# Kernel optimization log

Measured on AMD Instinct MI355X. Metric: run time of the kernel, lower is better.

## Reference

```python
import jax, jax.numpy as jnp
import numpy as np

B, T, D, V, L = 32, 1000, 768, 31, 200  # batch, frames, feat dim, vocab (blank=0), max target len
NEG = -1e30  # log-domain 'zero'


def setup_inputs() -> dict:
    key = jax.random.key(0)
    ks = jax.random.split(key, 5)
    pred = jax.random.normal(ks[0], (B, T, D), jnp.float32)
    targets = jax.random.randint(ks[1], (B * L,), 1, V)            # flat labels, blank(0) excluded
    input_lengths = jax.random.randint(ks[2], (B,), 800, T + 1)
    target_lengths = jax.random.randint(ks[3], (B,), 150, L + 1)
    W = jax.random.normal(ks[4], (V, D), jnp.float32) * 0.02       # ctc_head weight
    b = jnp.zeros((V,), jnp.float32)                               # ctc_head bias
    return dict(pred=pred, targets=targets, input_lengths=input_lengths,
                target_lengths=target_lengths, W=W, b=b)


def _ctc_loss(log_probs, tgt2d, in_len, tgt_len):
    """log_probs: (B,T,V); tgt2d: (B,L) padded labels; mean CTC loss (torch semantics,
    blank=0, reduction='mean', zero_infinity=True)."""
    Bv, Tv, _ = log_probs.shape
    Lv = tgt2d.shape[1]
    S = 2 * Lv + 1
    # extended label sequence: blank, l1, blank, l2, ..., blank
    ext = jnp.zeros((Bv, S), jnp.int32).at[:, 1::2].set(tgt2d.astype(jnp.int32))
    # gather log-probs of extended labels: (B,T,S)
    lp_ext = jnp.take_along_axis(log_probs, jnp.broadcast_to(ext[:, None, :], (Bv, Tv, S)), axis=2)
    prev2 = jnp.concatenate([jnp.full((Bv, 2), -1, jnp.int32), ext[:, :-2]], axis=1)
    skip = (jnp.arange(S)[None, :] >= 2) & (ext != 0) & (ext != prev2)
    in_len = in_len.astype(jnp.int32)

    alpha0 = (jnp.full((Bv, S), NEG, log_probs.dtype)
              .at[:, 0].set(lp_ext[:, 0, 0])
              .at[:, 1].set(lp_ext[:, 0, 1]))
    lp_seq = jnp.moveaxis(lp_ext, 1, 0)  # (T,B,S)

    def step(alpha, x):
        lp_t, t = x
        a1 = jnp.concatenate([jnp.full((Bv, 1), NEG, alpha.dtype), alpha[:, :-1]], axis=1)
        a2 = jnp.concatenate([jnp.full((Bv, 2), NEG, alpha.dtype), alpha[:, :-2]], axis=1)
        a2 = jnp.where(skip, a2, NEG)
        m = jnp.maximum(jnp.maximum(alpha, a1), a2)
        new = m + jnp.log(jnp.exp(alpha - m) + jnp.exp(a1 - m) + jnp.exp(a2 - m)) + lp_t
        alpha = jnp.where((t < in_len)[:, None], new, alpha)  # freeze past input_length
        return alpha, None

    alpha, _ = jax.lax.scan(step, alpha0, (lp_seq[1:], jnp.arange(1, Tv, dtype=jnp.int32)))
    # total log-prob: alpha at states 2*tl-1 and 2*tl
    idx = jnp.stack([2 * tgt_len - 1, 2 * tgt_len], axis=1).astype(jnp.int32)
    a_end = jnp.take_along_axis(alpha, idx, axis=1)  # (B,2)
    m = jnp.max(a_end, axis=1)
    nll = -(m + jnp.log(jnp.sum(jnp.exp(a_end - m[:, None]), axis=1)))
    nll = jnp.where(nll > 1e29, 0.0, nll)  # zero_infinity=True
    return jnp.mean(nll / tgt_len.astype(log_probs.dtype))  # torch 'mean' reduction


def reference(pred, targets, input_lengths, target_lengths, W, b):
    logits = jnp.einsum('btd,vd->btv', pred, W) + b      # ctc_head
    log_probs = jax.nn.log_softmax(logits, axis=-1)
    tgt2d = targets.reshape(B, L)
    loss = _ctc_loss(log_probs, tgt2d, input_lengths, target_lengths)
    return loss
```

## Files before the change

### kernel.cpp

```cpp
#include <hip/hip_runtime.h>
#include <hip/hip_bf16.h>
#include <cstdint>
#include <math.h>

#define B_DIM 32
#define T_DIM 1000
#define D_DIM 768
#define V_DIM 31
#define L_DIM 200
#define S_DIM 401
#define S_PAD 512
#define VSTRIDE 32

typedef __bf16 bf16x8 __attribute__((ext_vector_type(8)));
typedef float  f32x16 __attribute__((ext_vector_type(16)));
typedef float  f32x2  __attribute__((ext_vector_type(2)));
typedef __attribute__((address_space(3))) float lds_float;

#define SB() __builtin_amdgcn_sched_barrier(0)

__device__ __forceinline__ float shup1_f(float x) {
    int r = __builtin_amdgcn_update_dpp(0, __float_as_int(x), 0x138, 0xF, 0xF, true);
    return __int_as_float(r);
}
__device__ __forceinline__ int shup1_i(int x) {
    return __builtin_amdgcn_update_dpp(0, x, 0x138, 0xF, 0xF, true);
}

__global__ __launch_bounds__(256) void head_softmax_kernel(
    const float* __restrict__ pred,
    const float* __restrict__ W,
    const float* __restrict__ bias,
    float* __restrict__ probs)
{
    __shared__ float red[3][64][16];
    __shared__ float sm2[32][33];
    const int tid  = threadIdx.x;
    const int lane = tid & 63;
    const int w    = __builtin_amdgcn_readfirstlane(tid >> 6);
    const int col  = lane & 31;
    const int h    = lane >> 5;
    const int row  = blockIdx.x * 32 + col;
    const int vc   = (col < V_DIM) ? col : (V_DIM - 1);

    const float* pA = pred + (size_t)row * D_DIM + w * 192 + 8 * h;
    const float* pB = W + (size_t)vc * D_DIM + w * 192 + 8 * h;

    f32x16 acc;
#pragma unroll
    for (int i = 0; i < 16; ++i) acc[i] = 0.f;

#pragma unroll
    for (int kt = 0; kt < 12; ++kt) {
        const float4 a0 = *reinterpret_cast<const float4*>(pA + kt * 16);
        const float4 a1 = *reinterpret_cast<const float4*>(pA + kt * 16 + 4);
        const float4 b0 = *reinterpret_cast<const float4*>(pB + kt * 16);
        const float4 b1 = *reinterpret_cast<const float4*>(pB + kt * 16 + 4);
        bf16x8 af, bfr;
        af[0] = (__bf16)a0.x; af[1] = (__bf16)a0.y;
        af[2] = (__bf16)a0.z; af[3] = (__bf16)a0.w;
        af[4] = (__bf16)a1.x; af[5] = (__bf16)a1.y;
        af[6] = (__bf16)a1.z; af[7] = (__bf16)a1.w;
        bfr[0] = (__bf16)b0.x; bfr[1] = (__bf16)b0.y;
        bfr[2] = (__bf16)b0.z; bfr[3] = (__bf16)b0.w;
        bfr[4] = (__bf16)b1.x; bfr[5] = (__bf16)b1.y;
        bfr[6] = (__bf16)b1.z; bfr[7] = (__bf16)b1.w;
        acc = __builtin_amdgcn_mfma_f32_32x32x16_bf16(af, bfr, acc, 0, 0, 0);
    }

    if (w > 0) {
#pragma unroll
        for (int q = 0; q < 4; ++q)
            *reinterpret_cast<float4*>(&red[w - 1][lane][q * 4]) =
                make_float4(acc[q * 4], acc[q * 4 + 1], acc[q * 4 + 2], acc[q * 4 + 3]);
    }
    __syncthreads();
    if (w == 0) {
#pragma unroll
        for (int i = 0; i < 16; ++i)
            acc[i] += red[0][lane][i] + red[1][lane][i] + red[2][lane][i];
#pragma unroll
        for (int r = 0; r < 16; ++r) {
            const int rl = (r & 3) + 8 * (r >> 2) + 4 * h;
            sm2[rl][col] = acc[r];
        }
        if (lane < 32) {
            float lg[V_DIM];
            float m = -1e30f;
#pragma unroll
            for (int v = 0; v < V_DIM; ++v) {
                lg[v] = sm2[lane][v] + bias[v];
                m = fmaxf(m, lg[v]);
            }
            float e[32];
            float s = 0.f;
#pragma unroll
            for (int v = 0; v < V_DIM; ++v) { e[v] = __expf(lg[v] - m); s += e[v]; }
            const float inv = 1.0f / s;
#pragma unroll
            for (int v = 0; v < V_DIM; ++v) e[v] *= inv;
            e[31] = 0.f;
            float* op = probs + (size_t)(blockIdx.x * 32 + lane) * VSTRIDE;
#pragma unroll
            for (int q = 0; q < 8; ++q)
                *reinterpret_cast<float4*>(op + q * 4) =
                    *reinterpret_cast<float4*>(&e[q * 4]);
        }
    }
}

#define WTn(n) do { asm volatile("s_waitcnt lgkmcnt(" #n ")" ::: "memory"); SB(); } while (0)
#define VM8()  asm volatile("s_waitcnt vmcnt(8)" ::: "memory")
#define BARR() do { asm volatile("s_waitcnt lgkmcnt(0)" ::: "memory"); SB(); \
                    asm volatile("s_barrier" ::: "memory"); SB(); } while (0)
#define RD3(G, off) do { \
    asm volatile("ds_read_b32 %0, %1 offset:" #off : "=v"(G[0]) : "v"(va[0])); \
    asm volatile("ds_read_b32 %0, %1 offset:" #off : "=v"(G[1]) : "v"(va[1])); \
    asm volatile("ds_read_b32 %0, %1 offset:" #off : "=v"(G[2]) : "v"(va[2])); } while (0)
#define RDE(E, base, off) \
    asm volatile("ds_read_b64 %0, %1 offset:" #off : "=v"(E) : "v"(base))
#define WB(o0, o1) \
    asm volatile("ds_write2_b32 %0, %1, %2 offset0:" #o0 " offset1:" #o1 \
                 :: "v"(wcur), "v"(a[3]), "v"(z2) : "memory")

__global__ __launch_bounds__(128, 1) void ctc_alpha_kernel(
    const float* __restrict__ probs,
    const int* __restrict__ targets,
    const int* __restrict__ in_lens,
    const int* __restrict__ tgt_lens,
    float* __restrict__ out_nll)
{
    __shared__ float lbuf[4][16][VSTRIDE];
    __shared__ __align__(8) float bndb[3][16][2];
    __shared__ float trash[256];
    __shared__ float sal[S_PAD];

    const int b    = blockIdx.x;
    const int tid  = threadIdx.x;
    const int lane = tid & 63;
    const int w    = __builtin_amdgcn_readfirstlane(tid >> 6);
    const int Tin  = in_lens[b];
    const int tl   = tgt_lens[b];
    const int* tgt = targets + b * L_DIM;
    const float* __restrict__ prow = probs + (size_t)b * T_DIM * VSTRIDE;

    const int NS = Tin - 1;
    const int F  = NS >> 4;
    const int R  = NS & 15;

    int k0 = (w ? 128 : 0) + 2 * lane;
    int k1 = k0 + 1;
    if (k0 > L_DIM - 1) k0 = L_DIM - 1;
    if (k1 > L_DIM - 1) k1 = L_DIM - 1;
    const int loff0 = tgt[k0];
    const int loff1 = tgt[k1];
    const int k0m   = (k0 > 0) ? k0 - 1 : 0;
    const float m20 = (w == 0 && lane == 0) ? 0.f : ((loff0 != tgt[k0m]) ? 1.f : 0.f);
    const float m21 = (loff1 != tgt[k1 - 1]) ? 1.f : 0.f;

    const uint32_t lb_base  = (uint32_t)(uintptr_t)(lds_float*)&lbuf[0][0][0];
    const uint32_t bnd_base = (uint32_t)(uintptr_t)(lds_float*)&bndb[0][0][0];
    const uint32_t tr_base  = (uint32_t)(uintptr_t)(lds_float*)&trash[0];

    float a[4] = {0.f, 0.f, 0.f, 0.f};
    int   z2 = 0;
    const float fz = (lane == 0) ? 0.f : 1.0f;
    float f = fz;

    uint32_t va[3];
    va[0] = lb_base + (uint32_t)(loff0 * 4);
    va[1] = lb_base + (uint32_t)(loff1 * 4);
    va[2] = lb_base;

    float GA[3], GB[3], GC[3], GD[3];

    if (w == 0) {
        if (lane == 0) {
            a[0] = prow[0];
            a[1] = prow[loff0];
        }
        const uint32_t wsel = (lane == 63) ? bnd_base : (tr_base + (uint32_t)(lane * 8));
        uint32_t wcur = wsel;
        {
            const uint32_t winit = wsel + 256;
            asm volatile("ds_write2_b32 %0, %1, %2 offset0:30 offset1:31"
                         :: "v"(winit), "v"(a[3]), "v"(z2) : "memory");
        }

        auto ISSUE = [&](uint32_t slotbyte, int tbase) {
#pragma unroll
            for (int i = 0; i < 8; ++i) {
                int rowb = tbase + 2 * i;
                if (rowb > T_DIM - 2) rowb = T_DIM - 2;
                const float* src = prow + (size_t)rowb * VSTRIDE + lane;
                float* dst = &lbuf[0][0][0] + slotbyte / 4 + i * 64;
                __builtin_amdgcn_global_load_lds(
                    (const __attribute__((address_space(1))) void*)src,
                    (__attribute__((address_space(3))) void*)dst, 4, 0, 0);
            }
        };
        auto ST0 = [&](const float (&G)[3]) {
            const float s3p = shup1_f(a[3]);
            const float am1 = s3p * f;
            const float n0 = (a[0] + am1) * G[2];
            const float n1 = (a[1] + a[0] + m20 * am1) * G[0];
            const float n2 = (a[2] + a[1]) * G[2];
            const float n3 = (a[3] + a[2] + m21 * a[1]) * G[1];
            a[0] = n0; a[1] = n1; a[2] = n2; a[3] = n3;
        };
        auto REN0 = [&]() {
            const float mx = fmaxf(fmaxf(a[0], a[1]), fmaxf(a[2], a[3]));
            int e; (void)frexpf(mx, &e);
            const int zc = z2 + e;
            const int zp = shup1_i(zc);
            z2 = (mx > 0.f) ? zc : zp;
            a[0] = ldexpf(a[0], -e); a[1] = ldexpf(a[1], -e);
            a[2] = ldexpf(a[2], -e); a[3] = ldexpf(a[3], -e);
            const int dz = zp - z2;
            f = ldexpf(fz, dz);
        };

        uint32_t ro = 0, dsto = 4096;
        int tbi = 33;
        ISSUE(0, 1);
        ISSUE(2048, 17);
        VM8();
        RD3(GA, 0);
        RD3(GB, 128);

        for (int s = 0; s < F; ++s) {
            RD3(GC, 256);  WTn(8); ST0(GA);         WB(0, 1);
            RD3(GD, 384);  WTn(8); ST0(GB); REN0(); WB(2, 3);
            RD3(GA, 512);  WTn(8); ST0(GC);         WB(4, 5);
            RD3(GB, 640);  WTn(8); ST0(GD); REN0(); WB(6, 7);
            RD3(GC, 768);  WTn(8); ST0(GA);         WB(8, 9);
            RD3(GD, 896);  WTn(8); ST0(GB); REN0(); WB(10, 11);
            RD3(GA, 1024); WTn(8); ST0(GC);         WB(12, 13);
            RD3(GB, 1152); WTn(8); ST0(GD); REN0(); WB(14, 15);
            RD3(GC, 1280); WTn(8); ST0(GA);         WB(16, 17);
            RD3(GD, 1408); WTn(8); ST0(GB); REN0(); WB(18, 19);
            RD3(GA, 1536); WTn(8); ST0(GC);         WB(20, 21);
            RD3(GB, 1664); WTn(8); ST0(GD); REN0(); WB(22, 23);
            RD3(GC, 1792); WTn(8); ST0(GA);         WB(24, 25);
            RD3(GD, 1920); WTn(8); ST0(GB); REN0(); WB(26, 27);
            ro = (ro + 2048u) & 8191u;
            va[0] = lb_base + ro + (uint32_t)(loff0 * 4);
            va[1] = lb_base + ro + (uint32_t)(loff1 * 4);
            va[2] = lb_base + ro;
            ISSUE(dsto, tbi);
            dsto = (dsto + 2048u) & 8191u;
            tbi += 16;
            VM8();
            RD3(GA, 0);    WTn(8); ST0(GC);         WB(28, 29);
            RD3(GB, 128);  WTn(8); ST0(GD); REN0(); WB(30, 31);
            wcur = (wcur == wsel + 256u) ? wsel : wcur + 128u;
            BARR();
        }
        if (R > 0)  { RD3(GC, 256);  WTn(8); ST0(GA);         WB(0, 1); }
        if (R > 1)  { RD3(GD, 384);  WTn(8); ST0(GB); REN0(); WB(2, 3); }
        if (R > 2)  { RD3(GA, 512);  WTn(8); ST0(GC);         WB(4, 5); }
        if (R > 3)  { RD3(GB, 640);  WTn(8); ST0(GD); REN0(); WB(6, 7); }
        if (R > 4)  { RD3(GC, 768);  WTn(8); ST0(GA);         WB(8, 9); }
        if (R > 5)  { RD3(GD, 896);  WTn(8); ST0(GB); REN0(); WB(10, 11); }
        if (R > 6)  { RD3(GA, 1024); WTn(8); ST0(GC);         WB(12, 13); }
        if (R > 7)  { RD3(GB, 1152); WTn(8); ST0(GD); REN0(); WB(14, 15); }
        if (R > 8)  { RD3(GC, 1280); WTn(8); ST0(GA);         WB(16, 17); }
        if (R > 9)  { RD3(GD, 1408); WTn(8); ST0(GB); REN0(); WB(18, 19); }
        if (R > 10) { RD3(GA, 1536); WTn(8); ST0(GC);         WB(20, 21); }
        if (R > 11) { RD3(GB, 1664); WTn(8); ST0(GD); REN0(); WB(22, 23); }
        if (R > 12) { RD3(GC, 1792); WTn(8); ST0(GA);         WB(24, 25); }
        if (R > 13) { RD3(GD, 1920); WTn(8); ST0(GB); REN0(); WB(26, 27); }
        if (R > 14) { WTn(4); ST0(GC); WB(28, 29); }
        BARR();
        return;
    } else {
        const float fbz = (lane == 0) ? 1.0f : 0.f;
        f32x2 EA, EB, EC, ED;

        auto ST1 = [&](const float (&G)[3], const f32x2& E) {
            const float s3p = shup1_f(a[3]);
            float am1 = s3p * f;
            const int dzb = __float_as_int(E[1]) - z2;
            am1 = fmaf(E[0], ldexpf(fbz, dzb), am1);
            const float n0 = (a[0] + am1) * G[2];
            const float n1 = (a[1] + a[0] + m20 * am1) * G[0];
            const float n2 = (a[2] + a[1]) * G[2];
            const float n3 = (a[3] + a[2] + m21 * a[1]) * G[1];
            a[0] = n0; a[1] = n1; a[2] = n2; a[3] = n3;
        };
        auto REN1 = [&](const f32x2& E) {
            const float mx = fmaxf(fmaxf(a[0], a[1]), fmaxf(a[2], a[3]));
            int e; (void)frexpf(mx, &e);
            const int zc = z2 + e;
            int zp = shup1_i(zc);
            zp = (lane == 0) ? __float_as_int(E[1]) : zp;
            z2 = (mx > 0.f) ? zc : zp;
            a[0] = ldexpf(a[0], -e); a[1] = ldexpf(a[1], -e);
            a[2] = ldexpf(a[2], -e); a[3] = ldexpf(a[3], -e);
            const int dz = zp - z2;
            f = ldexpf(fz, dz);
        };

        uint32_t ro = 0;
        uint32_t cb = bnd_base, pb = bnd_base + 256u;
        BARR();
        for (int c = 0; c < F; ++c) {
            RD3(GA, 0);    RDE(EA, pb, 120);
            RD3(GB, 128);  RDE(EB, cb, 0);
            WTn(0);
            RD3(GC, 256);  RDE(EC, cb, 8);   WTn(8); ST1(GA, EA);
            RD3(GD, 384);  RDE(ED, cb, 16);  WTn(8); ST1(GB, EB); REN1(EB);
            RD3(GA, 512);  RDE(EA, cb, 24);  WTn(8); ST1(GC, EC);
            RD3(GB, 640);  RDE(EB, cb, 32);  WTn(8); ST1(GD, ED); REN1(ED);
            RD3(GC, 768);  RDE(EC, cb, 40);  WTn(8); ST1(GA, EA);
            RD3(GD, 896);  RDE(ED, cb, 48);  WTn(8); ST1(GB, EB); REN1(EB);
            RD3(GA, 1024); RDE(EA, cb, 56);  WTn(8); ST1(GC, EC);
            RD3(GB, 1152); RDE(EB, cb, 64);  WTn(8); ST1(GD, ED); REN1(ED);
            RD3(GC, 1280); RDE(EC, cb, 72);  WTn(8); ST1(GA, EA);
            RD3(GD, 1408); RDE(ED, cb, 80);  WTn(8); ST1(GB, EB); REN1(EB);
            RD3(GA, 1536); RDE(EA, cb, 88);  WTn(8); ST1(GC, EC);
            RD3(GB, 1664); RDE(EB, cb, 96);  WTn(8); ST1(GD, ED); REN1(ED);
            RD3(GC, 1792); RDE(EC, cb, 104); WTn(8); ST1(GA, EA);
            RD3(GD, 1920); RDE(ED, cb, 112); WTn(8); ST1(GB, EB); REN1(EB);
            WTn(4); ST1(GC, EC);
            WTn(0); ST1(GD, ED); REN1(ED);
            ro = (ro + 2048u) & 8191u;
            va[0] = lb_base + ro + (uint32_t)(loff0 * 4);
            va[1] = lb_base + ro + (uint32_t)(loff1 * 4);
            va[2] = lb_base + ro;
            pb = cb;
            cb = (cb == bnd_base + 256u) ? bnd_base : cb + 128u;
            BARR();
        }
        if (R > 0) {
            RD3(GA, 0);   RDE(EA, pb, 120);
            RD3(GB, 128); RDE(EB, cb, 0);
            WTn(0);
            RD3(GC, 256); RDE(EC, cb, 8); WTn(8); ST1(GA, EA);
        }
        if (R > 1)  { RD3(GD, 384);  RDE(ED, cb, 16);  WTn(8); ST1(GB, EB); REN1(EB); }
        if (R > 2)  { RD3(GA, 512);  RDE(EA, cb, 24);  WTn(8); ST1(GC, EC); }
        if (R > 3)  { RD3(GB, 640);  RDE(EB, cb, 32);  WTn(8); ST1(GD, ED); REN1(ED); }
        if (R > 4)  { RD3(GC, 768);  RDE(EC, cb, 40);  WTn(8); ST1(GA, EA); }
        if (R > 5)  { RD3(GD, 896);  RDE(ED, cb, 48);  WTn(8); ST1(GB, EB); REN1(EB); }
        if (R > 6)  { RD3(GA, 1024); RDE(EA, cb, 56);  WTn(8); ST1(GC, EC); }
        if (R > 7)  { RD3(GB, 1152); RDE(EB, cb, 64);  WTn(8); ST1(GD, ED); REN1(ED); }
        if (R > 8)  { RD3(GC, 1280); RDE(EC, cb, 72);  WTn(8); ST1(GA, EA); }
        if (R > 9)  { RD3(GD, 1408); RDE(ED, cb, 80);  WTn(8); ST1(GB, EB); REN1(EB); }
        if (R > 10) { RD3(GA, 1536); RDE(EA, cb, 88);  WTn(8); ST1(GC, EC); }
        if (R > 11) { RD3(GB, 1664); RDE(EB, cb, 96);  WTn(8); ST1(GD, ED); REN1(ED); }
        if (R > 12) { RD3(GC, 1792); RDE(EC, cb, 104); WTn(8); ST1(GA, EA); }
        if (R > 13) { RD3(GD, 1920); RDE(ED, cb, 112); WTn(8); ST1(GB, EB); REN1(EB); }
        if (R > 14) { WTn(4); ST1(GC, EC); }
        WTn(0);

        const float zln2 = (float)z2 * 0.69314718055994530942f;
        sal[256 + 4 * lane + 0] = __logf(a[0]) + zln2;
        sal[256 + 4 * lane + 1] = __logf(a[1]) + zln2;
        sal[256 + 4 * lane + 2] = __logf(a[2]) + zln2;
        sal[256 + 4 * lane + 3] = __logf(a[3]) + zln2;
        asm volatile("s_waitcnt lgkmcnt(0)" ::: "memory");
        SB();
        if (lane == 0) {
            const float x0 = sal[2 * tl - 1];
            const float x1 = sal[2 * tl];
            const float m  = fmaxf(x0, x1);
            float nll = -(m + __logf(__expf(x0 - m) + __expf(x1 - m)));
            if (!(nll < 1e29f)) nll = 0.f;
            out_nll[b] = nll / (float)tl;
        }
    }
}

__global__ void finalize_kernel(const float* __restrict__ nll, float* __restrict__ out)
{
    if (threadIdx.x == 0 && blockIdx.x == 0) {
        float s = 0.f;
        for (int i = 0; i < B_DIM; ++i) s += nll[i];
        out[0] = s * (1.0f / (float)B_DIM);
    }
}

extern "C" void kernel_launch(void* const* d_in, const int* in_sizes, int n_in,
                              void* d_out, int out_size, void* d_ws, size_t ws_size,
                              hipStream_t stream)
{
    const float* pred     = (const float*)d_in[0];
    const int*   targets  = (const int*)d_in[1];
    const int*   in_lens  = (const int*)d_in[2];
    const int*   tgt_lens = (const int*)d_in[3];
    const float* W        = (const float*)d_in[4];
    const float* bias     = (const float*)d_in[5];

    float* probs = (float*)d_ws;
    float* nll   = probs + (size_t)B_DIM * T_DIM * VSTRIDE;
    float* out   = (float*)d_out;

    head_softmax_kernel<<<(B_DIM * T_DIM) / 32, 256, 0, stream>>>(pred, W, bias, probs);
    ctc_alpha_kernel<<<B_DIM, 128, 0, stream>>>(probs, targets, in_lens, tgt_lens, nll);
    finalize_kernel<<<1, 64, 0, stream>>>(nll, out);
}
```

Baseline: 97.61 us.

## Fuse head-softmax and CTC alpha into one persistent kernel with flag handoff

Merges the projection/softmax kernel and the CTC recursion into a single launch. 224 worker blocks pull row tiles from an atomic work queue and publish per-tile ready flags, while 32 CTC blocks spin on those flags before streaming each time chunk. The goal is to overlap the serial alpha recursion with the GEMM/softmax and drop a kernel boundary. It adds a zeroing kernel, atomic polling and extra idle waves that only spin on barriers, and it depends on all CTC and worker blocks being resident at once to avoid deadlock.

```diff
diff --git a/kernel.cpp b/kernel.cpp
--- a/kernel.cpp
+++ b/kernel.cpp
@@ -11,6 +11,7 @@
 #define S_DIM 401
 #define S_PAD 512
 #define VSTRIDE 32
+#define NTASK 1024
 
 typedef __bf16 bf16x8 __attribute__((ext_vector_type(8)));
 typedef float  f32x16 __attribute__((ext_vector_type(16)));
@@ -25,88 +26,6 @@
 }
 __device__ __forceinline__ int shup1_i(int x) {
     return __builtin_amdgcn_update_dpp(0, x, 0x138, 0xF, 0xF, true);
-}
-
-__global__ __launch_bounds__(256) void head_softmax_kernel(
-    const float* __restrict__ pred,
-    const float* __restrict__ W,
-    const float* __restrict__ bias,
-    float* __restrict__ probs)
-{
-    __shared__ float red[3][64][16];
-    __shared__ float sm2[32][33];
-    const int tid  = threadIdx.x;
-    const int lane = tid & 63;
-    const int w    = __builtin_amdgcn_readfirstlane(tid >> 6);
-    const int col  = lane & 31;
-    const int h    = lane >> 5;
-    const int row  = blockIdx.x * 32 + col;
-    const int vc   = (col < V_DIM) ? col : (V_DIM - 1);
-
-    const float* pA = pred + (size_t)row * D_DIM + w * 192 + 8 * h;
-    const float* pB = W + (size_t)vc * D_DIM + w * 192 + 8 * h;
-
-    f32x16 acc;
-#pragma unroll
-    for (int i = 0; i < 16; ++i) acc[i] = 0.f;
-
-#pragma unroll
-    for (int kt = 0; kt < 12; ++kt) {
-        const float4 a0 = *reinterpret_cast<const float4*>(pA + kt * 16);
-        const float4 a1 = *reinterpret_cast<const float4*>(pA + kt * 16 + 4);
-        const float4 b0 = *reinterpret_cast<const float4*>(pB + kt * 16);
-        const float4 b1 = *reinterpret_cast<const float4*>(pB + kt * 16 + 4);
-        bf16x8 af, bfr;
-        af[0] = (__bf16)a0.x; af[1] = (__bf16)a0.y;
-        af[2] = (__bf16)a0.z; af[3] = (__bf16)a0.w;
-        af[4] = (__bf16)a1.x; af[5] = (__bf16)a1.y;
-        af[6] = (__bf16)a1.z; af[7] = (__bf16)a1.w;
-        bfr[0] = (__bf16)b0.x; bfr[1] = (__bf16)b0.y;
-        bfr[2] = (__bf16)b0.z; bfr[3] = (__bf16)b0.w;
-        bfr[4] = (__bf16)b1.x; bfr[5] = (__bf16)b1.y;
-        bfr[6] = (__bf16)b1.z; bfr[7] = (__bf16)b1.w;
-        acc = __builtin_amdgcn_mfma_f32_32x32x16_bf16(af, bfr, acc, 0, 0, 0);
-    }
-
-    if (w > 0) {
-#pragma unroll
-        for (int q = 0; q < 4; ++q)
-            *reinterpret_cast<float4*>(&red[w - 1][lane][q * 4]) =
-                make_float4(acc[q * 4], acc[q * 4 + 1], acc[q * 4 + 2], acc[q * 4 + 3]);
-    }
-    __syncthreads();
-    if (w == 0) {
-#pragma unroll
-        for (int i = 0; i < 16; ++i)
-            acc[i] += red[0][lane][i] + red[1][lane][i] + red[2][lane][i];
-#pragma unroll
-        for (int r = 0; r < 16; ++r) {
-            const int rl = (r & 3) + 8 * (r >> 2) + 4 * h;
-            sm2[rl][col] = acc[r];
-        }
-        if (lane < 32) {
-            float lg[V_DIM];
-            float m = -1e30f;
-#pragma unroll
-            for (int v = 0; v < V_DIM; ++v) {
-                lg[v] = sm2[lane][v] + bias[v];
-                m = fmaxf(m, lg[v]);
-            }
-            float e[32];
-            float s = 0.f;
-#pragma unroll
-            for (int v = 0; v < V_DIM; ++v) { e[v] = __expf(lg[v] - m); s += e[v]; }
-            const float inv = 1.0f / s;
-#pragma unroll
-            for (int v = 0; v < V_DIM; ++v) e[v] *= inv;
-            e[31] = 0.f;
-            float* op = probs + (size_t)(blockIdx.x * 32 + lane) * VSTRIDE;
-#pragma unroll
-            for (int q = 0; q < 8; ++q)
-                *reinterpret_cast<float4*>(op + q * 4) =
-                    *reinterpret_cast<float4*>(&e[q * 4]);
-        }
-    }
 }
 
 #define WTn(n) do { asm volatile("s_waitcnt lgkmcnt(" #n ")" ::: "memory"); SB(); } while (0)
@@ -123,22 +42,124 @@
     asm volatile("ds_write2_b32 %0, %1, %2 offset0:" #o0 " offset1:" #o1 \
                  :: "v"(wcur), "v"(a[3]), "v"(z2) : "memory")
 
-__global__ __launch_bounds__(128, 1) void ctc_alpha_kernel(
-    const float* __restrict__ probs,
+__global__ void zero_kernel(int* __restrict__ qf)
+{
+    for (int i = threadIdx.x; i < NTASK + 1; i += 256) qf[i] = 0;
+}
+
+__global__ __launch_bounds__(256) void fused_kernel(
+    const float* __restrict__ pred,
     const int* __restrict__ targets,
     const int* __restrict__ in_lens,
     const int* __restrict__ tgt_lens,
-    float* __restrict__ out_nll)
+    const float* __restrict__ W,
+    const float* __restrict__ bias,
+    float* __restrict__ probs,
+    float* __restrict__ out_nll,
+    int* __restrict__ queue,
+    int* __restrict__ flags)
 {
+    __shared__ float red[3][64][16];
+    __shared__ float sm2[32][33];
+    __shared__ int   taskS;
     __shared__ float lbuf[4][16][VSTRIDE];
     __shared__ __align__(8) float bndb[3][16][2];
     __shared__ float trash[256];
     __shared__ float sal[S_PAD];
 
-    const int b    = blockIdx.x;
     const int tid  = threadIdx.x;
     const int lane = tid & 63;
     const int w    = __builtin_amdgcn_readfirstlane(tid >> 6);
+
+    if (blockIdx.x >= 32) {
+        const int col = lane & 31;
+        const int h   = lane >> 5;
+        const int vc  = (col < V_DIM) ? col : (V_DIM - 1);
+        for (;;) {
+            if (tid == 0) taskS = atomicAdd(queue, 1);
+            __syncthreads();
+            const int task = taskS;
+            if (task >= NTASK) break;
+            const int b     = task & 31;
+            const int kk    = task >> 5;
+            const int rbase = b * T_DIM + kk * 32;
+            const int rmax  = b * T_DIM + T_DIM - 1;
+            int rowg = rbase + col;
+            if (rowg > rmax) rowg = rmax;
+
+            const float* pA = pred + (size_t)rowg * D_DIM + w * 192 + 8 * h;
+            const float* pB = W + (size_t)vc * D_DIM + w * 192 + 8 * h;
+
+            f32x16 acc;
+#pragma unroll
+            for (int i = 0; i < 16; ++i) acc[i] = 0.f;
+#pragma unroll
+            for (int kt = 0; kt < 12; ++kt) {
+                const float4 a0 = *reinterpret_cast<const float4*>(pA + kt * 16);
+                const float4 a1 = *reinterpret_cast<const float4*>(pA + kt * 16 + 4);
+                const float4 b0 = *reinterpret_cast<const float4*>(pB + kt * 16);
+                const float4 b1 = *reinterpret_cast<const float4*>(pB + kt * 16 + 4);
+                bf16x8 af, bfr;
+                af[0] = (__bf16)a0.x; af[1] = (__bf16)a0.y;
+                af[2] = (__bf16)a0.z; af[3] = (__bf16)a0.w;
+                af[4] = (__bf16)a1.x; af[5] = (__bf16)a1.y;
+                af[6] = (__bf16)a1.z; af[7] = (__bf16)a1.w;
+                bfr[0] = (__bf16)b0.x; bfr[1] = (__bf16)b0.y;
+                bfr[2] = (__bf16)b0.z; bfr[3] = (__bf16)b0.w;
+                bfr[4] = (__bf16)b1.x; bfr[5] = (__bf16)b1.y;
+                bfr[6] = (__bf16)b1.z; bfr[7] = (__bf16)b1.w;
+                acc = __builtin_amdgcn_mfma_f32_32x32x16_bf16(af, bfr, acc, 0, 0, 0);
+            }
+            if (w > 0) {
+#pragma unroll
+                for (int q = 0; q < 4; ++q)
+                    *reinterpret_cast<float4*>(&red[w - 1][lane][q * 4]) =
+                        make_float4(acc[q * 4], acc[q * 4 + 1], acc[q * 4 + 2], acc[q * 4 + 3]);
+            }
+            __syncthreads();
+            if (w == 0) {
+#pragma unroll
+                for (int i = 0; i < 16; ++i)
+                    acc[i] += red[0][lane][i] + red[1][lane][i] + red[2][lane][i];
+#pragma unroll
+                for (int r = 0; r < 16; ++r) {
+                    const int rl = (r & 3) + 8 * (r >> 2) + 4 * h;
+                    sm2[rl][col] = acc[r];
+                }
+                if (lane < 32 && rbase + lane <= rmax) {
+                    float lg[V_DIM];
+                    float m = -1e30f;
+#pragma unroll
+                    for (int v = 0; v < V_DIM; ++v) {
+                        lg[v] = sm2[lane][v] + bias[v];
+                        m = fmaxf(m, lg[v]);
+                    }
+                    float e[32];
+                    float s = 0.f;
+#pragma unroll
+                    for (int v = 0; v < V_DIM; ++v) { e[v] = __expf(lg[v] - m); s += e[v]; }
+                    const float inv = 1.0f / s;
+#pragma unroll
+                    for (int v = 0; v < V_DIM; ++v) e[v] *= inv;
+                    e[31] = 0.f;
+                    float* op = probs + (size_t)(rbase + lane) * VSTRIDE;
+#pragma unroll
+                    for (int q = 0; q < 8; ++q)
+                        *reinterpret_cast<float4*>(op + q * 4) =
+                            *reinterpret_cast<float4*>(&e[q * 4]);
+                }
+            }
+            if (tid == 0) {
+                __threadfence();
+                __hip_atomic_store(&flags[task], 1, __ATOMIC_RELEASE,
+                                   __HIP_MEMORY_SCOPE_AGENT);
+            }
+            __syncthreads();
+        }
+        return;
+    }
+
+    const int b    = blockIdx.x;
     const int Tin  = in_lens[b];
     const int tl   = tgt_lens[b];
     const int* tgt = targets + b * L_DIM;
@@ -147,6 +168,11 @@
     const int NS = Tin - 1;
     const int F  = NS >> 4;
     const int R  = NS & 15;
+
+    if (w >= 2) {
+        for (int i = 0; i <= F; ++i) asm volatile("s_barrier" ::: "memory");
+        return;
+    }
 
     int k0 = (w ? 128 : 0) + 2 * lane;
     int k1 = k0 + 1;
@@ -175,11 +201,28 @@
     float GA[3], GB[3], GC[3], GD[3];
 
     if (w == 0) {
+        int* bflags = flags + b * 32;
+        int pf = 0;
+        auto CONFIRM = [&](int need) {
+            if (pf <= need) {
+                do {
+                    while (__hip_atomic_load(&bflags[pf], __ATOMIC_RELAXED,
+                                             __HIP_MEMORY_SCOPE_AGENT) == 0)
+                        __builtin_amdgcn_s_sleep(16);
+                    ++pf;
+                } while (pf <= need);
+                (void)__hip_atomic_load(&bflags[pf - 1], __ATOMIC_ACQUIRE,
+                                        __HIP_MEMORY_SCOPE_AGENT);
+                SB();
+            }
+        };
+
+        CONFIRM(1);
         if (lane == 0) {
             a[0] = prow[0];
             a[1] = prow[loff0];
         }
-        const uint32_t wsel = (lane == 63) ? bnd_base : (tr_base + (uint32_t)(lane * 8));
+        const uint32_t wsel = (lane == 63) ? bnd_base : (tr_base + (uint32_t)(lane * 4));
         uint32_t wcur = wsel;
         {
             const uint32_t winit = wsel + 256;
@@ -247,6 +290,11 @@
             va[0] = lb_base + ro + (uint32_t)(loff0 * 4);
             va[1] = lb_base + ro + (uint32_t)(loff1 * 4);
             va[2] = lb_base + ro;
+            {
+                int need = (tbi + 15) >> 5;
+                if (need > 31) need = 31;
+                CONFIRM(need);
+            }
             ISSUE(dsto, tbi);
             dsto = (dsto + 2048u) & 8191u;
             tbi += 16;
@@ -394,9 +442,11 @@
 
     float* probs = (float*)d_ws;
     float* nll   = probs + (size_t)B_DIM * T_DIM * VSTRIDE;
+    int*   qf    = (int*)(nll + B_DIM);
     float* out   = (float*)d_out;
 
-    head_softmax_kernel<<<(B_DIM * T_DIM) / 32, 256, 0, stream>>>(pred, W, bias, probs);
-    ctc_alpha_kernel<<<B_DIM, 128, 0, stream>>>(probs, targets, in_lens, tgt_lens, nll);
+    zero_kernel<<<1, 256, 0, stream>>>(qf);
+    fused_kernel<<<256, 256, 0, stream>>>(pred, targets, in_lens, tgt_lens,
+                                          W, bias, probs, nll, qf, qf + 1);
     finalize_kernel<<<1, 64, 0, stream>>>(nll, out);
 }
```

Measured after the change: 170.8 us. 1.75x slower.

## Fuse CTC head softmax into alpha kernel with producer waves feeding LDS

Applied to the files above, without the earlier changes.

Removes the separate head+softmax kernel and the global probs buffer. Each batch block now has two producer waves that compute 16-row chunks of logits with MFMA, using a bf16 copy of W staged in LDS, then apply softmax and write probabilities straight into the LDS ring the alpha recursion reads. Barriers keep producers and the two consumer waves in lockstep. The aim is to drop the HBM round trip for probs and the extra launch. The cost is that the whole GEMM now runs on only 32 blocks, which may leave most CUs idle and become the bottleneck.

```diff
diff --git a/kernel.cpp b/kernel.cpp
--- a/kernel.cpp
+++ b/kernel.cpp
@@ -13,7 +13,7 @@
 #define VSTRIDE 32
 
 typedef __bf16 bf16x8 __attribute__((ext_vector_type(8)));
-typedef float  f32x16 __attribute__((ext_vector_type(16)));
+typedef float  f32x4  __attribute__((ext_vector_type(4)));
 typedef float  f32x2  __attribute__((ext_vector_type(2)));
 typedef __attribute__((address_space(3))) float lds_float;
 
@@ -27,90 +27,7 @@
     return __builtin_amdgcn_update_dpp(0, x, 0x138, 0xF, 0xF, true);
 }
 
-__global__ __launch_bounds__(256) void head_softmax_kernel(
-    const float* __restrict__ pred,
-    const float* __restrict__ W,
-    const float* __restrict__ bias,
-    float* __restrict__ probs)
-{
-    __shared__ float red[3][64][16];
-    __shared__ float sm2[32][33];
-    const int tid  = threadIdx.x;
-    const int lane = tid & 63;
-    const int w    = __builtin_amdgcn_readfirstlane(tid >> 6);
-    const int col  = lane & 31;
-    const int h    = lane >> 5;
-    const int row  = blockIdx.x * 32 + col;
-    const int vc   = (col < V_DIM) ? col : (V_DIM - 1);
-
-    const float* pA = pred + (size_t)row * D_DIM + w * 192 + 8 * h;
-    const float* pB = W + (size_t)vc * D_DIM + w * 192 + 8 * h;
-
-    f32x16 acc;
-#pragma unroll
-    for (int i = 0; i < 16; ++i) acc[i] = 0.f;
-
-#pragma unroll
-    for (int kt = 0; kt < 12; ++kt) {
-        const float4 a0 = *reinterpret_cast<const float4*>(pA + kt * 16);
-        const float4 a1 = *reinterpret_cast<const float4*>(pA + kt * 16 + 4);
-        const float4 b0 = *reinterpret_cast<const float4*>(pB + kt * 16);
-        const float4 b1 = *reinterpret_cast<const float4*>(pB + kt * 16 + 4);
-        bf16x8 af, bfr;
-        af[0] = (__bf16)a0.x; af[1] = (__bf16)a0.y;
-        af[2] = (__bf16)a0.z; af[3] = (__bf16)a0.w;
-        af[4] = (__bf16)a1.x; af[5] = (__bf16)a1.y;
-        af[6] = (__bf16)a1.z; af[7] = (__bf16)a1.w;
-        bfr[0] = (__bf16)b0.x; bfr[1] = (__bf16)b0.y;
-        bfr[2] = (__bf16)b0.z; bfr[3] = (__bf16)b0.w;
-        bfr[4] = (__bf16)b1.x; bfr[5] = (__bf16)b1.y;
-        bfr[6] = (__bf16)b1.z; bfr[7] = (__bf16)b1.w;
-        acc = __builtin_amdgcn_mfma_f32_32x32x16_bf16(af, bfr, acc, 0, 0, 0);
-    }
-
-    if (w > 0) {
-#pragma unroll
-        for (int q = 0; q < 4; ++q)
-            *reinterpret_cast<float4*>(&red[w - 1][lane][q * 4]) =
-                make_float4(acc[q * 4], acc[q * 4 + 1], acc[q * 4 + 2], acc[q * 4 + 3]);
-    }
-    __syncthreads();
-    if (w == 0) {
-#pragma unroll
-        for (int i = 0; i < 16; ++i)
-            acc[i] += red[0][lane][i] + red[1][lane][i] + red[2][lane][i];
-#pragma unroll
-        for (int r = 0; r < 16; ++r) {
-            const int rl = (r & 3) + 8 * (r >> 2) + 4 * h;
-            sm2[rl][col] = acc[r];
-        }
-        if (lane < 32) {
-            float lg[V_DIM];
-            float m = -1e30f;
-#pragma unroll
-            for (int v = 0; v < V_DIM; ++v) {
-                lg[v] = sm2[lane][v] + bias[v];
-                m = fmaxf(m, lg[v]);
-            }
-            float e[32];
-            float s = 0.f;
-#pragma unroll
-            for (int v = 0; v < V_DIM; ++v) { e[v] = __expf(lg[v] - m); s += e[v]; }
-            const float inv = 1.0f / s;
-#pragma unroll
-            for (int v = 0; v < V_DIM; ++v) e[v] *= inv;
-            e[31] = 0.f;
-            float* op = probs + (size_t)(blockIdx.x * 32 + lane) * VSTRIDE;
-#pragma unroll
-            for (int q = 0; q < 8; ++q)
-                *reinterpret_cast<float4*>(op + q * 4) =
-                    *reinterpret_cast<float4*>(&e[q * 4]);
-        }
-    }
-}
-
 #define WTn(n) do { asm volatile("s_waitcnt lgkmcnt(" #n ")" ::: "memory"); SB(); } while (0)
-#define VM8()  asm volatile("s_waitcnt vmcnt(8)" ::: "memory")
 #define BARR() do { asm volatile("s_waitcnt lgkmcnt(0)" ::: "memory"); SB(); \
                     asm volatile("s_barrier" ::: "memory"); SB(); } while (0)
 #define RD3(G, off) do { \
@@ -123,17 +40,23 @@
     asm volatile("ds_write2_b32 %0, %1, %2 offset0:" #o0 " offset1:" #o1 \
                  :: "v"(wcur), "v"(a[3]), "v"(z2) : "memory")
 
-__global__ __launch_bounds__(128, 1) void ctc_alpha_kernel(
-    const float* __restrict__ probs,
+__global__ __launch_bounds__(256, 1) void fused_kernel(
+    const float* __restrict__ pred,
     const int* __restrict__ targets,
     const int* __restrict__ in_lens,
     const int* __restrict__ tgt_lens,
+    const float* __restrict__ W,
+    const float* __restrict__ bias,
     float* __restrict__ out_nll)
 {
     __shared__ float lbuf[4][16][VSTRIDE];
     __shared__ __align__(8) float bndb[3][16][2];
     __shared__ float trash[256];
     __shared__ float sal[S_PAD];
+    __shared__ float row0b[VSTRIDE];
+    __shared__ __bf16 wlds[32][D_DIM];
+    __shared__ float biasl[32];
+    __shared__ float csta[2][16][33];
 
     const int b    = blockIdx.x;
     const int tid  = threadIdx.x;
@@ -142,11 +65,95 @@
     const int Tin  = in_lens[b];
     const int tl   = tgt_lens[b];
     const int* tgt = targets + b * L_DIM;
-    const float* __restrict__ prow = probs + (size_t)b * T_DIM * VSTRIDE;
+    const float* __restrict__ predb = pred + (size_t)b * T_DIM * D_DIM;
 
     const int NS = Tin - 1;
     const int F  = NS >> 4;
     const int R  = NS & 15;
+
+    float* lbp = &lbuf[0][0][0];
+
+    if (w >= 2) {
+        const int pidx = w - 2;
+        for (int i = lane; i < 32 * D_DIM; i += 64) {
+            const int r = i / D_DIM, k = i - r * D_DIM;
+            wlds[r][k] = (r < V_DIM) ? (__bf16)W[r * D_DIM + k] : (__bf16)0.f;
+        }
+        if (lane < 32) biasl[lane] = (lane < V_DIM) ? bias[lane] : 0.f;
+
+        const int cc = lane & 15;
+        const int h2 = lane >> 4;
+        float (*cs)[33] = csta[pidx];
+
+        auto PRODUCE = [&](int rbase, float* dstbase, bool only0) {
+            int arow = rbase + cc;
+            if (arow > T_DIM - 1) arow = T_DIM - 1;
+            const float* pA = predb + (size_t)arow * D_DIM + h2 * 8;
+            f32x4 c0, c1;
+#pragma unroll
+            for (int i = 0; i < 4; ++i) { c0[i] = 0.f; c1[i] = 0.f; }
+#pragma unroll
+            for (int kt = 0; kt < 24; ++kt) {
+                const float4 a0 = *reinterpret_cast<const float4*>(pA + kt * 32);
+                const float4 a1 = *reinterpret_cast<const float4*>(pA + kt * 32 + 4);
+                bf16x8 af;
+                af[0] = (__bf16)a0.x; af[1] = (__bf16)a0.y;
+                af[2] = (__bf16)a0.z; af[3] = (__bf16)a0.w;
+                af[4] = (__bf16)a1.x; af[5] = (__bf16)a1.y;
+                af[6] = (__bf16)a1.z; af[7] = (__bf16)a1.w;
+                const bf16x8 b0 = *reinterpret_cast<const bf16x8*>(
+                    &wlds[cc][h2 * 8 + kt * 32]);
+                const bf16x8 b1 = *reinterpret_cast<const bf16x8*>(
+                    &wlds[16 + cc][h2 * 8 + kt * 32]);
+                c0 = __builtin_amdgcn_mfma_f32_16x16x32_bf16(af, b0, c0, 0, 0, 0);
+                c1 = __builtin_amdgcn_mfma_f32_16x16x32_bf16(af, b1, c1, 0, 0, 0);
+            }
+#pragma unroll
+            for (int r = 0; r < 4; ++r) {
+                cs[h2 * 4 + r][cc]      = c0[r];
+                cs[h2 * 4 + r][16 + cc] = c1[r];
+            }
+            asm volatile("s_waitcnt lgkmcnt(0)" ::: "memory");
+            SB();
+            if (lane < 16 && (!only0 || lane == 0)) {
+                float lg[V_DIM];
+                float m = -1e30f;
+#pragma unroll
+                for (int v = 0; v < V_DIM; ++v) {
+                    lg[v] = cs[lane][v] + biasl[v];
+                    m = fmaxf(m, lg[v]);
+                }
+                float e[32];
+                float s = 0.f;
+#pragma unroll
+                for (int v = 0; v < V_DIM; ++v) { e[v] = __expf(lg[v] - m); s += e[v]; }
+                const float inv = 1.0f / s;
+#pragma unroll
+                for (int v = 0; v < V_DIM; ++v) e[v] *= inv;
+                e[31] = 0.f;
+                float* dst = dstbase + lane * VSTRIDE;
+#pragma unroll
+                for (int q = 0; q < 8; ++q)
+                    *reinterpret_cast<float4*>(dst + q * 4) =
+                        *reinterpret_cast<float4*>(&e[q * 4]);
+            }
+        };
+
+        if (pidx == 0) {
+            PRODUCE(0, row0b, true);
+            PRODUCE(1, lbp + 0 * 512, false);
+        } else {
+            PRODUCE(17, lbp + 1 * 512, false);
+        }
+        BARR();
+        for (int k = 1; k <= F + 1; ++k) {
+            const int c = k + 1;
+            if (c <= F && (c & 1) == pidx)
+                PRODUCE(16 * c + 1, lbp + (c & 3) * 512, false);
+            BARR();
+        }
+        return;
+    }
 
     int k0 = (w ? 128 : 0) + 2 * lane;
     int k1 = k0 + 1;
@@ -175,11 +182,12 @@
     float GA[3], GB[3], GC[3], GD[3];
 
     if (w == 0) {
+        BARR();
         if (lane == 0) {
-            a[0] = prow[0];
-            a[1] = prow[loff0];
-        }
-        const uint32_t wsel = (lane == 63) ? bnd_base : (tr_base + (uint32_t)(lane * 8));
+            a[0] = row0b[0];
+            a[1] = row0b[loff0];
+        }
+        const uint32_t wsel = (lane == 63) ? bnd_base : (tr_base + (uint32_t)(lane * 4));
         uint32_t wcur = wsel;
         {
             const uint32_t winit = wsel + 256;
@@ -187,18 +195,6 @@
                          :: "v"(winit), "v"(a[3]), "v"(z2) : "memory");
         }
 
-        auto ISSUE = [&](uint32_t slotbyte, int tbase) {
-#pragma unroll
-            for (int i = 0; i < 8; ++i) {
-                int rowb = tbase + 2 * i;
-                if (rowb > T_DIM - 2) rowb = T_DIM - 2;
-                const float* src = prow + (size_t)rowb * VSTRIDE + lane;
-                float* dst = &lbuf[0][0][0] + slotbyte / 4 + i * 64;
-                __builtin_amdgcn_global_load_lds(
-                    (const __attribute__((address_space(1))) void*)src,
-                    (__attribute__((address_space(3))) void*)dst, 4, 0, 0);
-            }
-        };
         auto ST0 = [&](const float (&G)[3]) {
             const float s3p = shup1_f(a[3]);
             const float am1 = s3p * f;
@@ -220,11 +216,7 @@
             f = ldexpf(fz, dz);
         };
 
-        uint32_t ro = 0, dsto = 4096;
-        int tbi = 33;
-        ISSUE(0, 1);
-        ISSUE(2048, 17);
-        VM8();
+        uint32_t ro = 0;
         RD3(GA, 0);
         RD3(GB, 128);
 
@@ -247,10 +239,6 @@
             va[0] = lb_base + ro + (uint32_t)(loff0 * 4);
             va[1] = lb_base + ro + (uint32_t)(loff1 * 4);
             va[2] = lb_base + ro;
-            ISSUE(dsto, tbi);
-            dsto = (dsto + 2048u) & 8191u;
-            tbi += 16;
-            VM8();
             RD3(GA, 0);    WTn(8); ST0(GC);         WB(28, 29);
             RD3(GB, 128);  WTn(8); ST0(GD); REN0(); WB(30, 31);
             wcur = (wcur == wsel + 256u) ? wsel : wcur + 128u;
@@ -303,6 +291,7 @@
 
         uint32_t ro = 0;
         uint32_t cb = bnd_base, pb = bnd_base + 256u;
+        BARR();
         BARR();
         for (int c = 0; c < F; ++c) {
             RD3(GA, 0);    RDE(EA, pb, 120);
@@ -392,11 +381,10 @@
     const float* W        = (const float*)d_in[4];
     const float* bias     = (const float*)d_in[5];
 
-    float* probs = (float*)d_ws;
-    float* nll   = probs + (size_t)B_DIM * T_DIM * VSTRIDE;
-    float* out   = (float*)d_out;
-
-    head_softmax_kernel<<<(B_DIM * T_DIM) / 32, 256, 0, stream>>>(pred, W, bias, probs);
-    ctc_alpha_kernel<<<B_DIM, 128, 0, stream>>>(probs, targets, in_lens, tgt_lens, nll);
+    float* nll = (float*)d_ws;
+    float* out = (float*)d_out;
+
+    fused_kernel<<<B_DIM, 256, 0, stream>>>(pred, targets, in_lens, tgt_lens,
+                                            W, bias, nll);
     finalize_kernel<<<1, 64, 0, stream>>>(nll, out);
 }
```

After: 309.4 us. +216.9%, slower.
